# Optimization experiments

Hardware: AMD Instinct MI355X
Metric: run time of the kernel (lower is better)

The kernel has to match this reference:

```python
import jax, jax.numpy as jnp
import numpy as np

SR = 44100.0
N_FFT = 2048
BANDS = 128
C_IN = 2
D_OUT = 128
B = 8
T = 512


def _hz_to_mel(f):
    # Slaney mel scale (librosa default, htk=False)
    f = np.asarray(f, dtype=np.float64)
    f_sp = 200.0 / 3.0
    min_log_hz = 1000.0
    min_log_mel = min_log_hz / f_sp  # 15.0
    logstep = np.log(6.4) / 27.0
    lin = f / f_sp
    log = min_log_mel + np.log(np.maximum(f, 1e-10) / min_log_hz) / logstep
    return np.where(f >= min_log_hz, log, lin)


def _mel_to_hz(m):
    m = np.asarray(m, dtype=np.float64)
    f_sp = 200.0 / 3.0
    min_log_mel = 15.0
    logstep = np.log(6.4) / 27.0
    lin = m * f_sp
    log = 1000.0 * np.exp(logstep * (m - min_log_mel))
    return np.where(m >= min_log_mel, log, lin)


def _mel_filters(sr, n_fft, n_mels):
    # librosa.filters.mel(..., norm=None, fmin=0, fmax=sr/2)
    F = n_fft // 2 + 1
    fftfreqs = np.linspace(0.0, sr / 2.0, F)
    mels = np.linspace(_hz_to_mel(0.0), _hz_to_mel(sr / 2.0), n_mels + 2)
    mel_f = _mel_to_hz(mels)
    fdiff = np.diff(mel_f)
    ramps = mel_f[:, None] - fftfreqs[None, :]
    lower = -ramps[:-2] / fdiff[:-1, None]
    upper = ramps[2:] / fdiff[1:, None]
    return np.maximum(0.0, np.minimum(lower, upper))  # (n_mels, F)


def _build_bands(sr, n_fft, bands_num):
    # Mirrors BandSplit.__init__: edge residual bands + per-band nonzero gather tables.
    F = n_fft // 2 + 1
    mb = _mel_filters(sr, n_fft, bands_num - 2)
    b0 = np.zeros(F)
    i = int(np.argmax(mb[0]))
    b0[:i] = 1.0 - mb[0, :i]
    bl = np.zeros(F)
    i = int(np.argmax(mb[-1]))
    bl[i:] = 1.0 - mb[-1, i:]
    melbanks = np.concatenate([b0[None, :], mb, bl[None, :]], axis=0)  # (K, F)
    ola = melbanks.sum(axis=0)  # (F,), ~1.0 everywhere
    idx_list = [np.nonzero(melbanks[k])[0] for k in range(bands_num)]
    W = max(len(ix) for ix in idx_list)  # max band width
    pad_idx = n_fft // 2
    idxs = np.full((bands_num, W), pad_idx, dtype=np.int32)
    vals = np.zeros((bands_num, W), dtype=np.float32)
    for k, ix in enumerate(idx_list):
        idxs[k, : len(ix)] = ix
        vals[k, : len(ix)] = melbanks[k, ix]
    mask = (vals != 0.0).astype(np.float32)
    return (idxs.reshape(-1), vals.reshape(-1), mask.reshape(-1),
            ola.astype(np.float32), W)


def setup_inputs() -> dict:
    key = jax.random.key(0)
    k_x, k_w1, k_b1, k_w2, k_b2 = jax.random.split(key, 5)
    idx_flat, mel_flat, mask_flat, ola, W = _build_bands(SR, N_FFT, BANDS)
    F = N_FFT // 2 + 1
    x = jax.random.normal(k_x, (B, C_IN, T, F), dtype=jnp.float32)
    i1 = W * C_IN
    bound1 = 1.0 / np.sqrt(i1)
    pre_w = jax.random.uniform(k_w1, (BANDS, i1, D_OUT), jnp.float32, -bound1, bound1)
    pre_b = jax.random.normal(k_b1, (BANDS, D_OUT), jnp.float32) * 0.01
    bound2 = 1.0 / np.sqrt(D_OUT)
    post_w = jax.random.uniform(k_w2, (BANDS, D_OUT, i1), jnp.float32, -bound2, bound2)
    post_b = jax.random.normal(k_b2, (BANDS, i1), jnp.float32) * 0.01
    return {
        "x": x,
        "pre_w": pre_w, "pre_b": pre_b,
        "post_w": post_w, "post_b": post_b,
        "mel_flat": jnp.asarray(mel_flat),
        "mask_flat": jnp.asarray(mask_flat),
        "ola_window": jnp.asarray(ola),
        "idx_flat": jnp.asarray(idx_flat),
    }


def reference(x, pre_w, pre_b, post_w, post_b, mel_flat, mask_flat, ola_window, idx_flat):
    Bn, C, Tn, Fq = x.shape
    K = pre_b.shape[0]
    W = pre_w.shape[1] // C
    # ---- transform: gather + mel weighting + per-band linear ----
    g = x[:, :, :, idx_flat] * (mel_flat * mask_flat)            # (b, c, t, K*W)
    g = g.reshape(Bn, C, Tn, K, W)                               # b c t k w
    g = g.transpose(0, 2, 3, 4, 1).reshape(Bn, Tn, K, W * C)     # b t k (w c)
    z = jnp.einsum('btki,kio->btko', g, pre_w) + pre_b           # (b, t, K, d)
    # ---- inverse_transform: per-band linear + masked scatter-add + OLA norm ----
    y = jnp.einsum('btkd,kdo->btko', z, post_w) + post_b         # (b, t, K, W*C)
    y = y.reshape(Bn, Tn, K, W, C)
    y = y.transpose(0, 4, 1, 2, 3).reshape(Bn, C, Tn, K * W)     # b c t (k w)
    y = y * mask_flat
    buf = jnp.zeros((Bn, C, Tn, Fq), dtype=x.dtype)
    buf = buf.at[:, :, :, idx_flat].add(y)                       # scatter_add over f
    return buf / ola_window
```

## Files before the change

kernel.cpp:

```cpp
#include <hip/hip_runtime.h>
#include <hip/hip_fp16.h>

typedef __attribute__((ext_vector_type(8))) short short8;
typedef __attribute__((ext_vector_type(4))) float f32x4;

constexpr int D_OUTC = 128;
constexpr int T_LEN  = 512;
constexpr int C_INC  = 2;
constexpr int F_BINS = 1025;
constexpr int N_BANDS= 128;
constexpr int MAX_W  = 80;
constexpr int SCAP   = 4224;

__device__ inline short8 cvt8(const float v[8]) {
  short8 h;
  #pragma unroll
  for (int j = 0; j < 8; ++j) {
    unsigned u = __float_as_uint(v[j]);
    unsigned r = u + 0x7FFFu + ((u >> 16) & 1u);
    h[j] = (short)(r >> 16);
  }
  return h;
}

__global__ void k_len(const float* __restrict__ mask, const int* __restrict__ idx, int W,
                      int* __restrict__ lenT, int* __restrict__ startT) {
  const int k = blockIdx.x;
  const int lane = threadIdx.x;
  int cnt = 0;
  for (int w = lane; w < W; w += 64) cnt += (mask[k * W + w] != 0.f) ? 1 : 0;
  #pragma unroll
  for (int s = 32; s > 0; s >>= 1) cnt += __shfl_xor(cnt, s, 64);
  if (lane == 0) { lenT[k] = cnt; startT[k] = idx[k * W]; }
}
__global__ void k_scan(const int* __restrict__ lenT, int* __restrict__ lenPT,
                       int* __restrict__ offT, int* __restrict__ permT) {
  const int k = threadIdx.x;
  int l = lenT[k];
  lenPT[k] = (l + 15) & ~15;
  __shared__ int sh[N_BANDS];
  __shared__ int sl[N_BANDS];
  sh[k] = 2 * l;
  sl[k] = l;
  __syncthreads();
  for (int s = 1; s < N_BANDS; s <<= 1) {
    int t = (k >= s) ? sh[k - s] : 0;
    __syncthreads();
    sh[k] += t;
    __syncthreads();
  }
  offT[k] = sh[k] - 2 * l;
  if (k == N_BANDS - 1) offT[N_BANDS] = sh[k];
  int rank = 0;
  for (int j = 0; j < N_BANDS; ++j)
    rank += (sl[j] > l) || (sl[j] == l && j < k);
  permT[rank] = k;
}
__global__ void k_inv2(const int* __restrict__ startT, const int* __restrict__ lenT,
                       const int* __restrict__ offT, int* __restrict__ inv) {
  int f = blockIdx.x * 256 + threadIdx.x;
  if (f >= F_BINS) return;
  int r0 = -1, r1 = -1, r2 = -1, r3 = -1;
  int n = 0;
  for (int k = 0; k < N_BANDS; ++k) {
    unsigned rel = (unsigned)(f - startT[k]);
    if (rel < (unsigned)lenT[k]) {
      int v = offT[k] + 2 * (int)rel;
      if (n == 0) r0 = v; else if (n == 1) r1 = v; else if (n == 2) r2 = v; else r3 = v;
      ++n;
    }
  }
  *(int4*)&inv[f * 4] = make_int4(r0, r1, r2, r3);
}

__global__ void prep_w1(const float* __restrict__ pre_w, const float* __restrict__ mel,
                        const float* __restrict__ mask, const int* __restrict__ lenPT,
                        unsigned short* __restrict__ hh,
                        int W, int i1, int K1PA) {
  const int band = blockIdx.y;
  const int ip = blockIdx.x * 32 + (threadIdx.x & 31);
  const int lp = lenPT[band];
  const int c  = (ip >= lp) ? 1 : 0;
  const int w  = ip - (c ? lp : 0);
  const bool live = (ip < 2 * lp) && (w < W);
  float s = 0.f; int row = 0;
  if (live) { s = mel[band * W + w] * mask[band * W + w]; row = 2 * w + c; }
  for (int d = (threadIdx.x >> 5); d < D_OUTC; d += 8) {
    float v = live ? s * pre_w[((size_t)band * i1 + row) * D_OUTC + d] : 0.f;
    unsigned u = __float_as_uint(v);
    unsigned r = u + 0x7FFFu + ((u >> 16) & 1u);
    hh[((size_t)(band * D_OUTC + d)) * K1PA + ip] = (unsigned short)(r >> 16);
  }
}

__global__ void prep_w2(const float* __restrict__ post_w, const float* __restrict__ post_b,
                        const float* __restrict__ mask,
                        const int* __restrict__ idx, const float* __restrict__ ola,
                        unsigned short* __restrict__ hh, float* __restrict__ postbS,
                        int W, int i1, int K1PA) {
  const int band = blockIdx.y;
  const int o  = blockIdx.x * 2 + (threadIdx.x >> 7);
  const int dd = threadIdx.x & 127;
  float s = 0.f;
  if (o < i1) {
    int w = o >> 1;
    float mk = mask[band * W + w];
    if (mk != 0.f) s = mk / ola[idx[band * W + w]];
  }
  float v = (o < i1) ? s * post_w[((size_t)band * D_OUTC + dd) * i1 + o] : 0.f;
  unsigned u = __float_as_uint(v);
  unsigned r = u + 0x7FFFu + ((u >> 16) & 1u);
  hh[((size_t)(band * K1PA + o)) * D_OUTC + dd] = (unsigned short)(r >> 16);
  if (dd == 0 && o < i1)
    postbS[band * i1 + o] = s * post_b[band * i1 + o];
}

__global__ __launch_bounds__(128, 4)
void bandsplit_main(const float* __restrict__ x,
                    const unsigned short* __restrict__ wB1h,
                    const unsigned short* __restrict__ wB2h,
                    const float* __restrict__ pre_b,
                    const float* __restrict__ postbS,
                    const int* __restrict__ lenT,
                    const int* __restrict__ lenPT,
                    const int* __restrict__ offT,
                    const int* __restrict__ startT,
                    const int* __restrict__ permT,
                    __half* __restrict__ y,
                    int i1, int K1PA, int nmt)
{
  const int bid  = blockIdx.x;
  const int band = permT[bid / nmt];
  const int mt   = bid - (bid / nmt) * nmt;

  const int lenv = lenT[band];
  if (lenv == 0) return;
  const int lp   = lenPT[band];
  const int nks  = lp >> 4;
  const int i1e  = 2 * lenv;
  const int nOT  = (i1e + 15) >> 4;
  const int offk = offT[band];
  const int strt = startT[band];

  const int mbase = mt * 64;
  const int b  = mbase >> 9;
  const int t0 = mbase & 511;
  const int tid  = threadIdx.x;
  const int lane = tid & 63;
  const int wid  = tid >> 6;
  const int lr = lane & 15, lk = lane >> 4;
  const int m0 = wid * 32;

  __shared__ float zAll[2][16 * 132];
  float* zw = zAll[wid];

  const float* xr0A = x + ((size_t)(b * C_INC) * T_LEN + (t0 + m0 + lr)) * F_BINS + strt;
  const float* xr0B = xr0A + (size_t)16 * F_BINS;
  const size_t xcs = (size_t)T_LEN * F_BINS;

  f32x4 a1A[8] = {}, a1B[8] = {};
  const unsigned short* b1h = wB1h + ((size_t)(band * D_OUTC) + lr) * K1PA;

  for (int ks = 0; ks < nks; ++ks) {
    const int i0 = ks * 32 + lk * 8;
    const int cs = (i0 >= lp) ? 1 : 0;
    const int w0 = i0 - (cs ? lp : 0);
    const float* xrA = xr0A + (cs ? xcs : 0) + w0;
    const float* xrB = xr0B + (cs ? xcs : 0) + w0;
    float xvA[8], xvB[8];
    if (w0 + 8 <= lenv) {
      float4 q0, q1, q2, q3;
      __builtin_memcpy(&q0, xrA,     16);
      __builtin_memcpy(&q1, xrA + 4, 16);
      __builtin_memcpy(&q2, xrB,     16);
      __builtin_memcpy(&q3, xrB + 4, 16);
      xvA[0]=q0.x; xvA[1]=q0.y; xvA[2]=q0.z; xvA[3]=q0.w;
      xvA[4]=q1.x; xvA[5]=q1.y; xvA[6]=q1.z; xvA[7]=q1.w;
      xvB[0]=q2.x; xvB[1]=q2.y; xvB[2]=q2.z; xvB[3]=q2.w;
      xvB[4]=q3.x; xvB[5]=q3.y; xvB[6]=q3.z; xvB[7]=q3.w;
    } else {
      #pragma unroll
      for (int j = 0; j < 8; ++j) {
        bool ok = (w0 + j < lenv);
        xvA[j] = ok ? xrA[j] : 0.f;
        xvB[j] = ok ? xrB[j] : 0.f;
      }
    }
    const short8 ahA = cvt8(xvA);
    const short8 ahB = cvt8(xvB);

    #pragma unroll
    for (int half = 0; half < 2; ++half) {
      short8 BH[4];
      #pragma unroll
      for (int t = 0; t < 4; ++t) {
        const int dt = half * 4 + t;
        BH[t] = *(const short8*)&b1h[(size_t)dt * 16 * K1PA + i0];
      }
      #pragma unroll
      for (int t = 0; t < 4; ++t) {
        const int dt = half * 4 + t;
        a1A[dt] = __builtin_amdgcn_mfma_f32_16x16x32_bf16(ahA, BH[t], a1A[dt], 0, 0, 0);
        a1B[dt] = __builtin_amdgcn_mfma_f32_16x16x32_bf16(ahB, BH[t], a1B[dt], 0, 0, 0);
      }
    }
  }

  float pbv[8];
  #pragma unroll
  for (int dt = 0; dt < 8; ++dt) pbv[dt] = pre_b[band * D_OUTC + dt * 16 + lr];

  short8 zhA[4], zhB[4];
  #pragma unroll
  for (int dt = 0; dt < 8; ++dt)
    #pragma unroll
    for (int r = 0; r < 4; ++r)
      zw[(lk * 4 + r) * 132 + dt * 16 + lr] = a1A[dt][r] + pbv[dt];
  __syncthreads();
  #pragma unroll
  for (int ks = 0; ks < 4; ++ks) {
    float zv[8];
    *(float4*)&zv[0] = *(const float4*)&zw[lr * 132 + ks * 32 + lk * 8];
    *(float4*)&zv[4] = *(const float4*)&zw[lr * 132 + ks * 32 + lk * 8 + 4];
    zhA[ks] = cvt8(zv);
  }
  __syncthreads();
  #pragma unroll
  for (int dt = 0; dt < 8; ++dt)
    #pragma unroll
    for (int r = 0; r < 4; ++r)
      zw[(lk * 4 + r) * 132 + dt * 16 + lr] = a1B[dt][r] + pbv[dt];
  __syncthreads();
  #pragma unroll
  for (int ks = 0; ks < 4; ++ks) {
    float zv[8];
    *(float4*)&zv[0] = *(const float4*)&zw[lr * 132 + ks * 32 + lk * 8];
    *(float4*)&zv[4] = *(const float4*)&zw[lr * 132 + ks * 32 + lk * 8 + 4];
    zhB[ks] = cvt8(zv);
  }

  const unsigned short* b2h = wB2h + ((size_t)(band * K1PA) + lr) * D_OUTC;
  for (int ot = 0; ot < nOT; ot += 2) {
    const bool has2 = (ot + 1 < nOT);
    short8 B0[4], B1[4];
    #pragma unroll
    for (int ks = 0; ks < 4; ++ks)
      B0[ks] = *(const short8*)&b2h[(size_t)ot * 16 * D_OUTC + ks * 32 + lk * 8];
    if (has2) {
      #pragma unroll
      for (int ks = 0; ks < 4; ++ks)
        B1[ks] = *(const short8*)&b2h[(size_t)(ot + 1) * 16 * D_OUTC + ks * 32 + lk * 8];
    }
    f32x4 aA0 = {}, aB0 = {}, aA1 = {}, aB1 = {};
    #pragma unroll
    for (int ks = 0; ks < 4; ++ks) {
      aA0 = __builtin_amdgcn_mfma_f32_16x16x32_bf16(zhA[ks], B0[ks], aA0, 0, 0, 0);
      aB0 = __builtin_amdgcn_mfma_f32_16x16x32_bf16(zhB[ks], B0[ks], aB0, 0, 0, 0);
    }
    if (has2) {
      #pragma unroll
      for (int ks = 0; ks < 4; ++ks) {
        aA1 = __builtin_amdgcn_mfma_f32_16x16x32_bf16(zhA[ks], B1[ks], aA1, 0, 0, 0);
        aB1 = __builtin_amdgcn_mfma_f32_16x16x32_bf16(zhB[ks], B1[ks], aB1, 0, 0, 0);
      }
    }
    {
      const int o = ot * 16 + lr;
      if (o < i1e) {
        const float pb = postbS[band * i1 + o];
        const size_t ybA = ((size_t)(b * T_LEN + t0 + m0 + lk * 4)) * SCAP + offk + o;
        const size_t ybB = ybA + (size_t)16 * SCAP;
        #pragma unroll
        for (int r = 0; r < 4; ++r) {
          y[ybA + (size_t)r * SCAP] = __float2half_rn(aA0[r] + pb);
          y[ybB + (size_t)r * SCAP] = __float2half_rn(aB0[r] + pb);
        }
      }
    }
    if (has2) {
      const int o = (ot + 1) * 16 + lr;
      if (o < i1e) {
        const float pb = postbS[band * i1 + o];
        const size_t ybA = ((size_t)(b * T_LEN + t0 + m0 + lk * 4)) * SCAP + offk + o;
        const size_t ybB = ybA + (size_t)16 * SCAP;
        #pragma unroll
        for (int r = 0; r < 4; ++r) {
          y[ybA + (size_t)r * SCAP] = __float2half_rn(aA1[r] + pb);
          y[ybB + (size_t)r * SCAP] = __float2half_rn(aB1[r] + pb);
        }
      }
    }
  }
}

__global__ __launch_bounds__(256, 8)
void k_merge(const __half* __restrict__ y, const int* __restrict__ inv,
             float* __restrict__ out, int nbt) {
  const size_t crow = (size_t)T_LEN * F_BINS;
  for (int row = blockIdx.x; row < nbt; row += gridDim.x) {
    const int t = row & 511;
    const int b = row >> 9;
    const size_t ybase = (size_t)row * SCAP;
    float* o0 = out + ((size_t)(b * C_INC) * T_LEN + t) * F_BINS;
    float* o1 = o0 + crow;
    for (int f = threadIdx.x; f < F_BINS; f += 256) {
      const int4 iv = *reinterpret_cast<const int4*>(&inv[f * 4]);
      float s0 = 0.f, s1 = 0.f;
      if (iv.x >= 0) {
        const __half2 h = *reinterpret_cast<const __half2*>(&y[ybase + iv.x]);
        s0 += __half2float(h.x); s1 += __half2float(h.y);
      }
      if (iv.y >= 0) {
        const __half2 h = *reinterpret_cast<const __half2*>(&y[ybase + iv.y]);
        s0 += __half2float(h.x); s1 += __half2float(h.y);
      }
      if (iv.z >= 0) {
        const __half2 h = *reinterpret_cast<const __half2*>(&y[ybase + iv.z]);
        s0 += __half2float(h.x); s1 += __half2float(h.y);
      }
      if (iv.w >= 0) {
        const __half2 h = *reinterpret_cast<const __half2*>(&y[ybase + iv.w]);
        s0 += __half2float(h.x); s1 += __half2float(h.y);
      }
      o0[f] = s0;
      o1[f] = s1;
    }
  }
}

#define TPB 256
constexpr int MT     = 32;
constexpr int MAX_I1 = 2 * MAX_W;
constexpr int MAX_I1P= (MAX_I1 + 31) & ~31;
constexpr int GSTR   = 36;

__global__ __launch_bounds__(TPB, 2)
void bandsplit_fused(const float* __restrict__ x,
                     const float* __restrict__ pre_w,
                     const float* __restrict__ pre_b,
                     const float* __restrict__ post_w,
                     const float* __restrict__ post_b,
                     const float* __restrict__ mel,
                     const float* __restrict__ mask,
                     const float* __restrict__ ola,
                     const int*   __restrict__ idx,
                     float* __restrict__ out,
                     int W)
{
    const int i1  = 2 * W;
    const int I1P = (i1 + 31) & ~31;
    const int k     = blockIdx.y;
    const int mbase = blockIdx.x * MT;
    const int b     = mbase / T_LEN;
    const int t0    = mbase % T_LEN;
    const int tid = threadIdx.x;
    const int td  = tid & 31;
    const int tm  = tid >> 5;

    __shared__ float gT[MAX_I1P * GSTR];
    __shared__ float zT[D_OUTC * GSTR];
    __shared__ float wS[32 * D_OUTC];
    __shared__ float s_preb[D_OUTC];
    __shared__ float s_postb[MAX_I1];
    __shared__ float s_melmask[MAX_W];
    __shared__ float s_mask[MAX_W];
    __shared__ float s_iola[MAX_W];
    __shared__ int   s_idx[MAX_W];

    for (int j = tid; j < W; j += TPB) {
        int   f  = idx[k * W + j];
        float mv = mel[k * W + j];
        float mk = mask[k * W + j];
        s_idx[j]     = f;
        s_melmask[j] = mv * mk;
        s_mask[j]    = mk;
        s_iola[j]    = 1.0f / ola[f];
    }
    for (int j = tid; j < D_OUTC; j += TPB) s_preb[j]  = pre_b[k * D_OUTC + j];
    for (int j = tid; j < i1;     j += TPB) s_postb[j] = post_b[k * i1 + j];
    for (int j = tid; j < I1P * GSTR; j += TPB) gT[j] = 0.f;
    __syncthreads();

    for (int j = tid; j < MT * i1; j += TPB) {
        int w  = j % W;
        int cm = j / W;
        int c  = cm & 1;
        int ml = cm >> 1;
        int f  = s_idx[w];
        float v = x[((b * C_INC + c) * T_LEN + (t0 + ml)) * F_BINS + f] * s_melmask[w];
        gT[(2 * w + c) * GSTR + ml] = v;
    }
    __syncthreads();

    float az[4][4] = {};
    for (int i0 = 0; i0 < I1P; i0 += 32) {
        for (int j = tid; j < 32 * D_OUTC; j += TPB) {
            int ii = j >> 7, d = j & 127;
            int i  = i0 + ii;
            wS[j] = (i < i1) ? pre_w[(k * i1 + i) * D_OUTC + d] : 0.f;
        }
        __syncthreads();
        #pragma unroll 8
        for (int ii = 0; ii < 32; ++ii) {
            const float4 wv = *reinterpret_cast<const float4*>(&wS[ii * D_OUTC + td * 4]);
            const float4 gv = *reinterpret_cast<const float4*>(&gT[(i0 + ii) * GSTR + tm * 4]);
            az[0][0] += gv.x * wv.x; az[0][1] += gv.x * wv.y; az[0][2] += gv.x * wv.z; az[0][3] += gv.x * wv.w;
            az[1][0] += gv.y * wv.x; az[1][1] += gv.y * wv.y; az[1][2] += gv.y * wv.z; az[1][3] += gv.y * wv.w;
            az[2][0] += gv.z * wv.x; az[2][1] += gv.z * wv.y; az[2][2] += gv.z * wv.z; az[2][3] += gv.z * wv.w;
            az[3][0] += gv.w * wv.x; az[3][1] += gv.w * wv.y; az[3][2] += gv.w * wv.z; az[3][3] += gv.w * wv.w;
        }
        __syncthreads();
    }
    #pragma unroll
    for (int jj = 0; jj < 4; ++jj) {
        int d = td * 4 + jj;
        float bb = s_preb[d];
        #pragma unroll
        for (int r = 0; r < 4; ++r)
            zT[d * GSTR + tm * 4 + r] = az[r][jj] + bb;
    }
    __syncthreads();

    const int NOG = (i1 + 127) >> 7;
    for (int og = 0; og < NOG; ++og) {
        float ay[4][4] = {};
        for (int d0 = 0; d0 < D_OUTC; d0 += 32) {
            for (int j = tid; j < 32 * D_OUTC; j += TPB) {
                int dd = j >> 7, oo = j & 127;
                int o  = og * 128 + oo;
                wS[j] = (o < i1) ? post_w[(k * D_OUTC + d0 + dd) * i1 + o] : 0.f;
            }
            __syncthreads();
            #pragma unroll 8
            for (int dd = 0; dd < 32; ++dd) {
                const float4 wv = *reinterpret_cast<const float4*>(&wS[dd * D_OUTC + td * 4]);
                const float4 zv = *reinterpret_cast<const float4*>(&zT[(d0 + dd) * GSTR + tm * 4]);
                ay[0][0] += zv.x * wv.x; ay[0][1] += zv.x * wv.y; ay[0][2] += zv.x * wv.z; ay[0][3] += zv.x * wv.w;
                ay[1][0] += zv.y * wv.x; ay[1][1] += zv.y * wv.y; ay[1][2] += zv.y * wv.z; ay[1][3] += zv.y * wv.w;
                ay[2][0] += zv.z * wv.x; ay[2][1] += zv.z * wv.y; ay[2][2] += zv.z * wv.z; ay[2][3] += zv.z * wv.w;
                ay[3][0] += zv.w * wv.x; ay[3][1] += zv.w * wv.y; ay[3][2] += zv.w * wv.z; ay[3][3] += zv.w * wv.w;
            }
            __syncthreads();
        }
        #pragma unroll
        for (int jj = 0; jj < 4; ++jj) {
            int o = og * 128 + td * 4 + jj;
            if (o < i1) {
                int w = o >> 1, c = o & 1;
                float mk = s_mask[w];
                if (mk != 0.f) {
                    int f = s_idx[w];
                    float scale = mk * s_iola[w];
                    float bb = s_postb[o];
                    #pragma unroll
                    for (int r = 0; r < 4; ++r) {
                        int ml = tm * 4 + r;
                        float val = (ay[r][jj] + bb) * scale;
                        atomicAdd(&out[((b * C_INC + c) * T_LEN + (t0 + ml)) * F_BINS + f], val);
                    }
                }
            }
        }
    }
}

__global__ void bandsplit_naive(const float* __restrict__ x,
                                const float* __restrict__ pre_w,
                                const float* __restrict__ pre_b,
                                const float* __restrict__ post_w,
                                const float* __restrict__ post_b,
                                const float* __restrict__ mel,
                                const float* __restrict__ mask,
                                const float* __restrict__ ola,
                                const int*   __restrict__ idx,
                                float* __restrict__ out,
                                int W)
{
    const int i1 = 2 * W;
    extern __shared__ float sh[];
    float* g = sh;
    float* z = sh + i1;
    const int m = blockIdx.x, k = blockIdx.y;
    const int b = m / T_LEN, t = m % T_LEN;
    const int tid = threadIdx.x;
    for (int j = tid; j < i1; j += 128) {
        int w = j >> 1, c = j & 1;
        int f = idx[k * W + w];
        g[j] = x[((b * C_INC + c) * T_LEN + t) * F_BINS + f] * mel[k * W + w] * mask[k * W + w];
    }
    __syncthreads();
    {
        int d = tid;
        float a = pre_b[k * D_OUTC + d];
        for (int i = 0; i < i1; ++i) a += g[i] * pre_w[(k * i1 + i) * D_OUTC + d];
        z[d] = a;
    }
    __syncthreads();
    for (int o = tid; o < i1; o += 128) {
        int w = o >> 1, c = o & 1;
        float mk = mask[k * W + w];
        if (mk == 0.f) continue;
        float a = post_b[k * i1 + o];
        for (int d = 0; d < D_OUTC; ++d) a += z[d] * post_w[(k * D_OUTC + d) * i1 + o];
        int f = idx[k * W + w];
        atomicAdd(&out[((b * C_INC + c) * T_LEN + t) * F_BINS + f], a * mk / ola[f]);
    }
}

extern "C" void kernel_launch(void* const* d_in, const int* in_sizes, int n_in,
                              void* d_out, int out_size, void* d_ws, size_t ws_size,
                              hipStream_t stream) {
    const float* x      = (const float*)d_in[0];
    const float* pre_w  = (const float*)d_in[1];
    const float* pre_b  = (const float*)d_in[2];
    const float* post_w = (const float*)d_in[3];
    const float* post_b = (const float*)d_in[4];
    const float* mel    = (const float*)d_in[5];
    const float* mask   = (const float*)d_in[6];
    const float* ola    = (const float*)d_in[7];
    const int*   idxp   = (const int*)d_in[8];
    float* out = (float*)d_out;

    const int W  = in_sizes[8] / N_BANDS;
    const int i1 = 2 * W;
    const int Mrows = in_sizes[0] / (C_INC * F_BINS);
    const int K1PA = 2 * ((W + 15) & ~15);

    const size_t S1 = (size_t)N_BANDS * D_OUTC * K1PA;
    const size_t wbytes   = 4 * S1;
    const size_t pbs_off  = (wbytes + 15) & ~(size_t)15;
    const size_t inv_off  = (pbs_off + (size_t)N_BANDS * i1 * 4 + 15) & ~(size_t)15;
    const size_t len_off  = inv_off + (size_t)F_BINS * 4 * 4;
    const size_t lenp_off = len_off + N_BANDS * 4;
    const size_t offt_off = lenp_off + N_BANDS * 4;
    const size_t strt_off = offt_off + (N_BANDS + 1) * 4;
    const size_t perm_off = strt_off + N_BANDS * 4;
    const size_t y_off    = (perm_off + N_BANDS * 4 + 255) & ~(size_t)255;
    const size_t need     = y_off + (size_t)Mrows * SCAP * sizeof(__half);

    if (W <= MAX_W && (Mrows % 64) == 0 && (Mrows % T_LEN) == 0 && ws_size >= need) {
        char* ws = (char*)d_ws;
        unsigned short* wB1h = (unsigned short*)ws;
        unsigned short* wB2h = wB1h + S1;
        float* postbS = (float*)(ws + pbs_off);
        int* inv   = (int*)(ws + inv_off);
        int* lenT  = (int*)(ws + len_off);
        int* lenPT = (int*)(ws + lenp_off);
        int* offT  = (int*)(ws + offt_off);
        int* startT= (int*)(ws + strt_off);
        int* permT = (int*)(ws + perm_off);
        __half* y  = (__half*)(ws + y_off);

        k_len<<<N_BANDS, 64, 0, stream>>>(mask, idxp, W, lenT, startT);
        k_scan<<<1, N_BANDS, 0, stream>>>(lenT, lenPT, offT, permT);
        dim3 g1(K1PA / 32, N_BANDS);
        prep_w1<<<g1, 256, 0, stream>>>(pre_w, mel, mask, lenPT, wB1h, W, i1, K1PA);
        dim3 g2(K1PA / 2, N_BANDS);
        prep_w2<<<g2, 256, 0, stream>>>(post_w, post_b, mask, idxp, ola, wB2h, postbS,
                                        W, i1, K1PA);
        k_inv2<<<(F_BINS + 255) / 256, 256, 0, stream>>>(startT, lenT, offT, inv);
        const int nmt = Mrows / 64;
        bandsplit_main<<<nmt * N_BANDS, 128, 0, stream>>>(x, wB1h, wB2h,
                                                 pre_b, postbS, lenT, lenPT, offT, startT,
                                                 permT, y, i1, K1PA, nmt);
        k_merge<<<4096, 256, 0, stream>>>(y, inv, out, Mrows);
        return;
    }

    hipMemsetAsync(d_out, 0, (size_t)out_size * sizeof(float), stream);
    if (W <= MAX_W && (Mrows % MT) == 0) {
        dim3 grid(Mrows / MT, N_BANDS);
        bandsplit_fused<<<grid, TPB, 0, stream>>>(x, pre_w, pre_b, post_w, post_b,
                                                  mel, mask, ola, idxp, out, W);
    } else {
        dim3 grid(Mrows, N_BANDS);
        size_t shmem = (size_t)(2 * W + D_OUTC) * sizeof(float);
        bandsplit_naive<<<grid, 128, shmem, stream>>>(x, pre_w, pre_b, post_w, post_b,
                                                      mel, mask, ola, idxp, out, W);
    }
}
```

Before: 120.0 us.

## Split first GEMM into two D passes and stage z as bf16 in LDS

The first band GEMM now runs in two passes of 64 output columns, so only 8 accumulator tiles are live instead of 16. The intermediate z is written to shared memory as bf16 with a wider stride, and the second GEMM reads its A operands directly from LDS instead of holding them in registers. The second GEMM also handles one output tile per iteration instead of two. The goal is lower register pressure so occupancy can rise (launch bounds raised from 4 to 5), at the cost of re-reading x in both passes and extra LDS reads.

Result: slower. 132.2 us (+10.2%).

```diff
diff --git a/kernel.cpp b/kernel.cpp
--- a/kernel.cpp
+++ b/kernel.cpp
@@ -11,15 +11,17 @@
 constexpr int N_BANDS= 128;
 constexpr int MAX_W  = 80;
 constexpr int SCAP   = 4224;
-
+constexpr int ZSTRU  = 136;
+
+__device__ inline unsigned short bf16r(float f) {
+  unsigned u = __float_as_uint(f);
+  unsigned r = u + 0x7FFFu + ((u >> 16) & 1u);
+  return (unsigned short)(r >> 16);
+}
 __device__ inline short8 cvt8(const float v[8]) {
   short8 h;
   #pragma unroll
-  for (int j = 0; j < 8; ++j) {
-    unsigned u = __float_as_uint(v[j]);
-    unsigned r = u + 0x7FFFu + ((u >> 16) & 1u);
-    h[j] = (short)(r >> 16);
-  }
+  for (int j = 0; j < 8; ++j) h[j] = (short)bf16r(v[j]);
   return h;
 }
 
@@ -87,9 +89,7 @@
   if (live) { s = mel[band * W + w] * mask[band * W + w]; row = 2 * w + c; }
   for (int d = (threadIdx.x >> 5); d < D_OUTC; d += 8) {
     float v = live ? s * pre_w[((size_t)band * i1 + row) * D_OUTC + d] : 0.f;
-    unsigned u = __float_as_uint(v);
-    unsigned r = u + 0x7FFFu + ((u >> 16) & 1u);
-    hh[((size_t)(band * D_OUTC + d)) * K1PA + ip] = (unsigned short)(r >> 16);
+    hh[((size_t)(band * D_OUTC + d)) * K1PA + ip] = bf16r(v);
   }
 }
 
@@ -108,14 +108,12 @@
     if (mk != 0.f) s = mk / ola[idx[band * W + w]];
   }
   float v = (o < i1) ? s * post_w[((size_t)band * D_OUTC + dd) * i1 + o] : 0.f;
-  unsigned u = __float_as_uint(v);
-  unsigned r = u + 0x7FFFu + ((u >> 16) & 1u);
-  hh[((size_t)(band * K1PA + o)) * D_OUTC + dd] = (unsigned short)(r >> 16);
+  hh[((size_t)(band * K1PA + o)) * D_OUTC + dd] = bf16r(v);
   if (dd == 0 && o < i1)
     postbS[band * i1 + o] = s * post_b[band * i1 + o];
 }
 
-__global__ __launch_bounds__(128, 4)
+__global__ __launch_bounds__(128, 5)
 void bandsplit_main(const float* __restrict__ x,
                     const unsigned short* __restrict__ wB1h,
                     const unsigned short* __restrict__ wB2h,
@@ -151,143 +149,95 @@
   const int lr = lane & 15, lk = lane >> 4;
   const int m0 = wid * 32;
 
-  __shared__ float zAll[2][16 * 132];
-  float* zw = zAll[wid];
+  __shared__ unsigned short zAll[2][32 * ZSTRU];
+  unsigned short* zw = zAll[wid];
 
   const float* xr0A = x + ((size_t)(b * C_INC) * T_LEN + (t0 + m0 + lr)) * F_BINS + strt;
   const float* xr0B = xr0A + (size_t)16 * F_BINS;
   const size_t xcs = (size_t)T_LEN * F_BINS;
 
-  f32x4 a1A[8] = {}, a1B[8] = {};
-  const unsigned short* b1h = wB1h + ((size_t)(band * D_OUTC) + lr) * K1PA;
-
-  for (int ks = 0; ks < nks; ++ks) {
-    const int i0 = ks * 32 + lk * 8;
-    const int cs = (i0 >= lp) ? 1 : 0;
-    const int w0 = i0 - (cs ? lp : 0);
-    const float* xrA = xr0A + (cs ? xcs : 0) + w0;
-    const float* xrB = xr0B + (cs ? xcs : 0) + w0;
-    float xvA[8], xvB[8];
-    if (w0 + 8 <= lenv) {
-      float4 q0, q1, q2, q3;
-      __builtin_memcpy(&q0, xrA,     16);
-      __builtin_memcpy(&q1, xrA + 4, 16);
-      __builtin_memcpy(&q2, xrB,     16);
-      __builtin_memcpy(&q3, xrB + 4, 16);
-      xvA[0]=q0.x; xvA[1]=q0.y; xvA[2]=q0.z; xvA[3]=q0.w;
-      xvA[4]=q1.x; xvA[5]=q1.y; xvA[6]=q1.z; xvA[7]=q1.w;
-      xvB[0]=q2.x; xvB[1]=q2.y; xvB[2]=q2.z; xvB[3]=q2.w;
-      xvB[4]=q3.x; xvB[5]=q3.y; xvB[6]=q3.z; xvB[7]=q3.w;
-    } else {
-      #pragma unroll
-      for (int j = 0; j < 8; ++j) {
-        bool ok = (w0 + j < lenv);
-        xvA[j] = ok ? xrA[j] : 0.f;
-        xvB[j] = ok ? xrB[j] : 0.f;
-      }
-    }
-    const short8 ahA = cvt8(xvA);
-    const short8 ahB = cvt8(xvB);
-
-    #pragma unroll
-    for (int half = 0; half < 2; ++half) {
+  #pragma unroll
+  for (int dpass = 0; dpass < 2; ++dpass) {
+    f32x4 aA[4] = {}, aB[4] = {};
+    const unsigned short* b1p = wB1h + ((size_t)(band * D_OUTC + dpass * 64) + lr) * K1PA;
+
+    for (int ks = 0; ks < nks; ++ks) {
+      const int i0 = ks * 32 + lk * 8;
+      const int cs = (i0 >= lp) ? 1 : 0;
+      const int w0 = i0 - (cs ? lp : 0);
+      const float* xrA = xr0A + (cs ? xcs : 0) + w0;
+      const float* xrB = xr0B + (cs ? xcs : 0) + w0;
+      float xvA[8], xvB[8];
+      if (w0 + 8 <= lenv) {
+        float4 q0, q1, q2, q3;
+        __builtin_memcpy(&q0, xrA,     16);
+        __builtin_memcpy(&q1, xrA + 4, 16);
+        __builtin_memcpy(&q2, xrB,     16);
+        __builtin_memcpy(&q3, xrB + 4, 16);
+        xvA[0]=q0.x; xvA[1]=q0.y; xvA[2]=q0.z; xvA[3]=q0.w;
+        xvA[4]=q1.x; xvA[5]=q1.y; xvA[6]=q1.z; xvA[7]=q1.w;
+        xvB[0]=q2.x; xvB[1]=q2.y; xvB[2]=q2.z; xvB[3]=q2.w;
+        xvB[4]=q3.x; xvB[5]=q3.y; xvB[6]=q3.z; xvB[7]=q3.w;
+      } else {
+        #pragma unroll
+        for (int j = 0; j < 8; ++j) {
+          bool ok = (w0 + j < lenv);
+          xvA[j] = ok ? xrA[j] : 0.f;
+          xvB[j] = ok ? xrB[j] : 0.f;
+        }
+      }
+      const short8 ahA = cvt8(xvA);
+      const short8 ahB = cvt8(xvB);
+
       short8 BH[4];
       #pragma unroll
-      for (int t = 0; t < 4; ++t) {
-        const int dt = half * 4 + t;
-        BH[t] = *(const short8*)&b1h[(size_t)dt * 16 * K1PA + i0];
-      }
+      for (int t = 0; t < 4; ++t)
+        BH[t] = *(const short8*)&b1p[(size_t)t * 16 * K1PA + i0];
       #pragma unroll
       for (int t = 0; t < 4; ++t) {
-        const int dt = half * 4 + t;
-        a1A[dt] = __builtin_amdgcn_mfma_f32_16x16x32_bf16(ahA, BH[t], a1A[dt], 0, 0, 0);
-        a1B[dt] = __builtin_amdgcn_mfma_f32_16x16x32_bf16(ahB, BH[t], a1B[dt], 0, 0, 0);
-      }
-    }
-  }
-
-  float pbv[8];
-  #pragma unroll
-  for (int dt = 0; dt < 8; ++dt) pbv[dt] = pre_b[band * D_OUTC + dt * 16 + lr];
-
-  short8 zhA[4], zhB[4];
-  #pragma unroll
-  for (int dt = 0; dt < 8; ++dt)
+        aA[t] = __builtin_amdgcn_mfma_f32_16x16x32_bf16(ahA, BH[t], aA[t], 0, 0, 0);
+        aB[t] = __builtin_amdgcn_mfma_f32_16x16x32_bf16(ahB, BH[t], aB[t], 0, 0, 0);
+      }
+    }
+
     #pragma unroll
-    for (int r = 0; r < 4; ++r)
-      zw[(lk * 4 + r) * 132 + dt * 16 + lr] = a1A[dt][r] + pbv[dt];
+    for (int t = 0; t < 4; ++t) {
+      const int d = dpass * 64 + t * 16 + lr;
+      const float pb = pre_b[band * D_OUTC + d];
+      #pragma unroll
+      for (int r = 0; r < 4; ++r) {
+        const int m = lk * 4 + r;
+        zw[m * ZSTRU + d]        = bf16r(aA[t][r] + pb);
+        zw[(16 + m) * ZSTRU + d] = bf16r(aB[t][r] + pb);
+      }
+    }
+  }
+
   __syncthreads();
-  #pragma unroll
-  for (int ks = 0; ks < 4; ++ks) {
-    float zv[8];
-    *(float4*)&zv[0] = *(const float4*)&zw[lr * 132 + ks * 32 + lk * 8];
-    *(float4*)&zv[4] = *(const float4*)&zw[lr * 132 + ks * 32 + lk * 8 + 4];
-    zhA[ks] = cvt8(zv);
-  }
-  __syncthreads();
-  #pragma unroll
-  for (int dt = 0; dt < 8; ++dt)
-    #pragma unroll
-    for (int r = 0; r < 4; ++r)
-      zw[(lk * 4 + r) * 132 + dt * 16 + lr] = a1B[dt][r] + pbv[dt];
-  __syncthreads();
-  #pragma unroll
-  for (int ks = 0; ks < 4; ++ks) {
-    float zv[8];
-    *(float4*)&zv[0] = *(const float4*)&zw[lr * 132 + ks * 32 + lk * 8];
-    *(float4*)&zv[4] = *(const float4*)&zw[lr * 132 + ks * 32 + lk * 8 + 4];
-    zhB[ks] = cvt8(zv);
-  }
 
   const unsigned short* b2h = wB2h + ((size_t)(band * K1PA) + lr) * D_OUTC;
-  for (int ot = 0; ot < nOT; ot += 2) {
-    const bool has2 = (ot + 1 < nOT);
-    short8 B0[4], B1[4];
+  for (int ot = 0; ot < nOT; ++ot) {
+    short8 B0[4];
     #pragma unroll
     for (int ks = 0; ks < 4; ++ks)
       B0[ks] = *(const short8*)&b2h[(size_t)ot * 16 * D_OUTC + ks * 32 + lk * 8];
-    if (has2) {
-      #pragma unroll
-      for (int ks = 0; ks < 4; ++ks)
-        B1[ks] = *(const short8*)&b2h[(size_t)(ot + 1) * 16 * D_OUTC + ks * 32 + lk * 8];
-    }
-    f32x4 aA0 = {}, aB0 = {}, aA1 = {}, aB1 = {};
+    f32x4 aA = {}, aB = {};
     #pragma unroll
     for (int ks = 0; ks < 4; ++ks) {
-      aA0 = __builtin_amdgcn_mfma_f32_16x16x32_bf16(zhA[ks], B0[ks], aA0, 0, 0, 0);
-      aB0 = __builtin_amdgcn_mfma_f32_16x16x32_bf16(zhB[ks], B0[ks], aB0, 0, 0, 0);
-    }
-    if (has2) {
+      const short8 zA = *(const short8*)&zw[lr * ZSTRU + ks * 32 + lk * 8];
+      const short8 zB = *(const short8*)&zw[(16 + lr) * ZSTRU + ks * 32 + lk * 8];
+      aA = __builtin_amdgcn_mfma_f32_16x16x32_bf16(zA, B0[ks], aA, 0, 0, 0);
+      aB = __builtin_amdgcn_mfma_f32_16x16x32_bf16(zB, B0[ks], aB, 0, 0, 0);
+    }
+    const int o = ot * 16 + lr;
+    if (o < i1e) {
+      const float pb = postbS[band * i1 + o];
+      const size_t ybA = ((size_t)(b * T_LEN + t0 + m0 + lk * 4)) * SCAP + offk + o;
+      const size_t ybB = ybA + (size_t)16 * SCAP;
       #pragma unroll
-      for (int ks = 0; ks < 4; ++ks) {
-        aA1 = __builtin_amdgcn_mfma_f32_16x16x32_bf16(zhA[ks], B1[ks], aA1, 0, 0, 0);
-        aB1 = __builtin_amdgcn_mfma_f32_16x16x32_bf16(zhB[ks], B1[ks], aB1, 0, 0, 0);
-      }
-    }
-    {
-      const int o = ot * 16 + lr;
-      if (o < i1e) {
-        const float pb = postbS[band * i1 + o];
-        const size_t ybA = ((size_t)(b * T_LEN + t0 + m0 + lk * 4)) * SCAP + offk + o;
-        const size_t ybB = ybA + (size_t)16 * SCAP;
-        #pragma unroll
-        for (int r = 0; r < 4; ++r) {
-          y[ybA + (size_t)r * SCAP] = __float2half_rn(aA0[r] + pb);
-          y[ybB + (size_t)r * SCAP] = __float2half_rn(aB0[r] + pb);
-        }
-      }
-    }
-    if (has2) {
-      const int o = (ot + 1) * 16 + lr;
-      if (o < i1e) {
-        const float pb = postbS[band * i1 + o];
-        const size_t ybA = ((size_t)(b * T_LEN + t0 + m0 + lk * 4)) * SCAP + offk + o;
-        const size_t ybB = ybA + (size_t)16 * SCAP;
-        #pragma unroll
-        for (int r = 0; r < 4; ++r) {
-          y[ybA + (size_t)r * SCAP] = __float2half_rn(aA1[r] + pb);
-          y[ybB + (size_t)r * SCAP] = __float2half_rn(aB1[r] + pb);
-        }
+      for (int r = 0; r < 4; ++r) {
+        y[ybA + (size_t)r * SCAP] = __float2half_rn(aA[r] + pb);
+        y[ybB + (size_t)r * SCAP] = __float2half_rn(aB[r] + pb);
       }
     }
   }
```
